# Kernel tuning notes

Hardware: AMD Instinct MI355X
Metric: run time of the kernel (lower is better)

## Reference

```python
import jax, jax.numpy as jnp
import numpy as np

H, W = 1024, 2048
NUM_POS_MAX, NUM_TOTAL = 32, 128
POS_THR, NEG_THR = 0.5, 0.5
B, G, R = 8, 256, 16384
N = R + G  # rois + appended gt boxes per image


def _xy2cxcy(xy):
    # NOTE: original code halves wh (divides by 2.0) -- kept faithfully.
    return jnp.concatenate([(xy[..., 2:] + xy[..., :2]) / 2.0,
                            (xy[..., 2:] - xy[..., :2]) / 2.0], axis=-1)


def _encode(gt_cxcy, anc_cxcy):
    tg_cxy = (gt_cxcy[..., :2] - anc_cxcy[..., :2]) / anc_cxcy[..., 2:]
    tg_wh = jnp.log(gt_cxcy[..., 2:] / anc_cxcy[..., 2:])
    return jnp.concatenate([tg_cxy, tg_wh], axis=-1)


def _rank(key_vals):
    # rank of each element when sorted ascending (stable)
    return jnp.argsort(jnp.argsort(key_vals))


def _sample_one(gt_bbox, gt_label, roi, rp, rn):
    scale = jnp.array([W, H, W, H], dtype=roi.dtype)
    allroi = jnp.concatenate([roi, gt_bbox / scale], axis=0)  # (N,4)
    # dense IoU matrix (N,G) -- the memory-bound core
    lb = jnp.maximum(allroi[:, None, :2], gt_bbox[None, :, :2])
    ub = jnp.minimum(allroi[:, None, 2:], gt_bbox[None, :, 2:])
    whi = jnp.clip(ub - lb, 0.0)
    inter = whi[..., 0] * whi[..., 1]
    a1 = jnp.clip((allroi[:, 2] - allroi[:, 0]) * (allroi[:, 3] - allroi[:, 1]), 0.0)[:, None]
    a2 = jnp.clip((gt_bbox[:, 2] - gt_bbox[:, 0]) * (gt_bbox[:, 3] - gt_bbox[:, 1]), 0.0)[None, :]
    iou = inter / (a1 + a2 - inter)
    iou_max = iou.max(axis=1)
    iou_argmax = iou.argmax(axis=1)
    label_all = gt_label[iou_argmax] + 1

    pos_mask = iou_max >= POS_THR
    neg_mask = (iou_max < NEG_THR) & (iou_max >= 0.0)
    num_pos = jnp.minimum(pos_mask.sum(), NUM_POS_MAX)
    num_neg = NUM_TOTAL - num_pos
    # random-subset selection via random-key ranking (replaces torch.randperm)
    pos_rank = _rank(jnp.where(pos_mask, rp, jnp.inf))
    neg_rank = _rank(jnp.where(neg_mask, rn, jnp.inf))
    sel_pos = pos_mask & (pos_rank < num_pos)
    sel_neg = neg_mask & (neg_rank < num_neg)
    # positives occupy slots [0,num_pos), negatives slots [num_pos,NUM_TOTAL)
    slot = jnp.where(sel_pos, pos_rank, jnp.where(sel_neg, num_pos + neg_rank, NUM_TOTAL))
    sampled_ids = jnp.zeros((NUM_TOTAL,), jnp.int32).at[slot].set(
        jnp.arange(N, dtype=jnp.int32), mode='drop')

    label = jnp.where(jnp.arange(NUM_TOTAL) < num_pos,
                      label_all[sampled_ids], 0).astype(jnp.int32)
    target_bbox = gt_bbox[iou_argmax][sampled_ids]
    sampled_roi = allroi[sampled_ids]
    std = jnp.array([0.1, 0.1, 0.2, 0.2], dtype=roi.dtype)
    encoded = _encode(_xy2cxcy(target_bbox), _xy2cxcy(sampled_roi)) / std
    return label, encoded, sampled_roi


def setup_inputs() -> dict:
    key = jax.random.key(0)
    ks = jax.random.split(key, 7)
    sxy = jnp.array([W, H], jnp.float32)
    gt_x1y1 = jax.random.uniform(ks[0], (B, G, 2)) * 0.8 * sxy
    gt_wh = jax.random.uniform(ks[1], (B, G, 2)) * 0.15 * sxy + 2.0
    gt_bboxes = jnp.concatenate([gt_x1y1, gt_x1y1 + gt_wh], axis=-1)
    gt_labels = jax.random.randint(ks[2], (B, G), 0, 80)
    r_x1y1 = jax.random.uniform(ks[3], (B, R, 2)) * 0.8
    r_wh = jax.random.uniform(ks[4], (B, R, 2)) * 0.15 + 0.002
    rois = jnp.concatenate([r_x1y1, r_x1y1 + r_wh], axis=-1)
    rand_pos = jax.random.uniform(ks[5], (B, N))
    rand_neg = jax.random.uniform(ks[6], (B, N))
    return {"gt_bboxes": gt_bboxes, "gt_labels": gt_labels, "rois": rois,
            "rand_pos": rand_pos, "rand_neg": rand_neg}


def reference(gt_bboxes, gt_labels, rois, rand_pos, rand_neg):
    labels, bboxes, sampled_rois = jax.vmap(_sample_one)(
        gt_bboxes, gt_labels, rois, rand_pos, rand_neg)
    return labels, bboxes, sampled_rois
```

## Files before the change

kernel.cpp:

```cpp
#include <hip/hip_runtime.h>
#include <stdint.h>

#define HH 1024
#define WW 2048
#define GG 256
#define RRN 16384
#define NN 16640
#define NV (NN / 4)
#define BB 8
#define NUM_POS_MAX 32
#define NUM_TOTAL 128
#define CAP 1024
#define SEL_T 1024

__global__ __launch_bounds__(256) void iou_kernel(const float* __restrict__ gt,
                                                  const float* __restrict__ rois,
                                                  uint32_t* __restrict__ codes) {
#pragma clang fp contract(off)
    __shared__ float4 sg[GG];
    __shared__ float sa2[GG];
    int b = blockIdx.x / 65;
    int chunk = blockIdx.x % 65;
    int tid = threadIdx.x;

    float4 g = reinterpret_cast<const float4*>(gt)[b * GG + tid];
    sg[tid] = g;
    sa2[tid] = fmaxf((g.z - g.x) * (g.w - g.y), 0.0f);
    __syncthreads();

    int i = chunk * 256 + tid;
    float4 rb;
    if (i < RRN) {
        rb = reinterpret_cast<const float4*>(rois)[b * RRN + i];
    } else {
        float4 gp = sg[i - RRN];
        rb = make_float4(gp.x / (float)WW, gp.y / (float)HH,
                         gp.z / (float)WW, gp.w / (float)HH);
    }
    float a1 = fmaxf((rb.z - rb.x) * (rb.w - rb.y), 0.0f);

    float best = -1.0f;
    int bestj = 0;
    for (int j = 0; j < GG; ++j) {
        float4 gj = sg[j];
        float lx = fmaxf(rb.x, gj.x);
        float ly = fmaxf(rb.y, gj.y);
        float ux = fminf(rb.z, gj.z);
        float uy = fminf(rb.w, gj.w);
        float iw = fmaxf(ux - lx, 0.0f);
        float ih = fmaxf(uy - ly, 0.0f);
        float inter = iw * ih;
        float denom = (a1 + sa2[j]) - inter;
        float iou = inter / denom;
        if (iou > best) { best = iou; bestj = j; }
    }

    bool pos = (best >= 0.5f);
    codes[b * NN + i] = (uint32_t)bestj | (pos ? 0x10000u : 0u);
}

__device__ __forceinline__ void write_sample(int b, int s, int mi, int np,
                                             const float* __restrict__ gt,
                                             const int* __restrict__ gl,
                                             const float* __restrict__ rois,
                                             const uint32_t* __restrict__ codes,
                                             float* __restrict__ out) {
#pragma clang fp contract(off)
    uint32_t code = codes[b * NN + mi];
    int amax = (int)(code & 0xFFFFu);
    int label = (s < np) ? (gl[b * GG + amax] + 1) : 0;

    float4 tb = reinterpret_cast<const float4*>(gt)[b * GG + amax];
    float4 ar;
    if (mi < RRN) {
        ar = reinterpret_cast<const float4*>(rois)[b * RRN + mi];
    } else {
        float4 gp = reinterpret_cast<const float4*>(gt)[b * GG + (mi - RRN)];
        ar = make_float4(gp.x / (float)WW, gp.y / (float)HH,
                         gp.z / (float)WW, gp.w / (float)HH);
    }

    float acx = (ar.z + ar.x) / 2.0f, acy = (ar.w + ar.y) / 2.0f;
    float aw  = (ar.z - ar.x) / 2.0f, ah  = (ar.w - ar.y) / 2.0f;
    float gcx = (tb.z + tb.x) / 2.0f, gcy = (tb.w + tb.y) / 2.0f;
    float gw  = (tb.z - tb.x) / 2.0f, gh  = (tb.w - tb.y) / 2.0f;

    float e0 = ((gcx - acx) / aw) / 0.1f;
    float e1 = ((gcy - acy) / ah) / 0.1f;
    float e2 = logf(gw / aw) / 0.2f;
    float e3 = logf(gh / ah) / 0.2f;

    int gid = b * NUM_TOTAL + s;
    out[gid] = (float)label;
    float* eo = out + BB * NUM_TOTAL + gid * 4;
    eo[0] = e0; eo[1] = e1; eo[2] = e2; eo[3] = e3;
    float* ro = out + BB * NUM_TOTAL + BB * NUM_TOTAL * 4 + gid * 4;
    ro[0] = ar.x; ro[1] = ar.y; ro[2] = ar.z; ro[3] = ar.w;
}

__global__ __launch_bounds__(SEL_T) void select_kernel(const uint32_t* __restrict__ codes,
                                                       const float* __restrict__ rp,
                                                       const float* __restrict__ rn,
                                                       const float* __restrict__ gt,
                                                       const int* __restrict__ gl,
                                                       const float* __restrict__ rois,
                                                       float* __restrict__ out) {
    __shared__ unsigned hist[1024];
    __shared__ uint32_t cbits[CAP];
    __shared__ int cidx[CAP];
    __shared__ int s_pc, s_cnt, s_k, s_np, s_p, s_total;

    int b = blockIdx.x >> 1;
    int t = blockIdx.x & 1;
    int tid = threadIdx.x;
    const float* rnd = (t == 0) ? rp : rn;
    const uint4* c4p = reinterpret_cast<const uint4*>(codes + b * NN);
    const float4* r4p = reinterpret_cast<const float4*>(rnd + b * NN);

    if (tid == 0) { s_pc = 0; s_cnt = 0; }
    __syncthreads();

    unsigned cutoff = 1000;
    for (int attempt = 0; attempt < 2; ++attempt) {
        hist[tid] = 0u;
        if (tid == 0) s_p = -1;
        __syncthreads();

        int myPos = 0;
        for (int v = tid; v < NV; v += SEL_T) {
            uint4 c4 = c4p[v];
            float4 r4 = r4p[v];
            uint32_t cc[4] = {c4.x, c4.y, c4.z, c4.w};
            float rr[4] = {r4.x, r4.y, r4.z, r4.w};
#pragma unroll
            for (int e = 0; e < 4; ++e) {
                bool isPos = (cc[e] & 0x10000u) != 0u;
                myPos += isPos ? 1 : 0;
                bool m = (t == 0) ? isPos : !isPos;
                if (m) {
                    unsigned bin = __float_as_uint(rr[e]) >> 20;
                    if (bin < cutoff) atomicAdd(&hist[bin], 1u);
                }
            }
        }
        if (attempt == 0) {
            for (int o = 32; o; o >>= 1) myPos += __shfl_down(myPos, o, 64);
            if ((tid & 63) == 0) atomicAdd(&s_pc, myPos);
        }
        __syncthreads();

        for (int off = 1; off < 1024; off <<= 1) {
            unsigned v = (tid >= off) ? hist[tid - off] : 0u;
            __syncthreads();
            hist[tid] += v;
            __syncthreads();
        }

        if (tid == 0) {
            int pc = s_pc;
            int np_ = min(pc, NUM_POS_MAX);
            int k = (t == 0) ? np_ : min(NN - pc, NUM_TOTAL - np_);
            s_np = np_;
            s_k = k;
            s_total = (int)hist[1023];
        }
        __syncthreads();

        int k = s_k;
        if (k > 0 && (int)hist[tid] >= k && (tid == 0 || (int)hist[tid - 1] < k))
            s_p = tid;
        __syncthreads();

        if (s_k == 0 || s_total >= s_k) break;
        cutoff = 1024;
    }

    int p = s_p;
    int k = s_k;
    int np_ = s_np;

    if (p >= 0) {
        for (int v = tid; v < NV; v += SEL_T) {
            uint4 c4 = c4p[v];
            float4 r4 = r4p[v];
            uint32_t cc[4] = {c4.x, c4.y, c4.z, c4.w};
            float rr[4] = {r4.x, r4.y, r4.z, r4.w};
#pragma unroll
            for (int e = 0; e < 4; ++e) {
                bool isPos = (cc[e] & 0x10000u) != 0u;
                bool m = (t == 0) ? isPos : !isPos;
                if (m) {
                    uint32_t bits = __float_as_uint(rr[e]);
                    if ((int)(bits >> 20) <= p) {
                        int ix = atomicAdd(&s_cnt, 1);
                        if (ix < CAP) { cbits[ix] = bits; cidx[ix] = v * 4 + e; }
                    }
                }
            }
        }
    }
    __syncthreads();

    int c = min(s_cnt, CAP);
    for (int ci = tid; ci < c; ci += SEL_T) {
        uint32_t mb = cbits[ci];
        int mi = cidx[ci];
        int r = 0;
        for (int j = 0; j < c; ++j) {
            uint32_t ob = cbits[j];
            r += ((ob < mb) || (ob == mb && cidx[j] < mi)) ? 1 : 0;
        }
        if (r < k) {
            int s = (t == 0) ? r : (np_ + r);
            write_sample(b, s, mi, np_, gt, gl, rois, codes, out);
        }
    }

    if (t == 1) {
        for (int s = np_ + k + tid; s < NUM_TOTAL; s += SEL_T)
            write_sample(b, s, 0, np_, gt, gl, rois, codes, out);
    }
}

extern "C" void kernel_launch(void* const* d_in, const int* in_sizes, int n_in,
                              void* d_out, int out_size, void* d_ws, size_t ws_size,
                              hipStream_t stream) {
    const float* gt   = (const float*)d_in[0];
    const int*   gl   = (const int*)d_in[1];
    const float* rois = (const float*)d_in[2];
    const float* rp   = (const float*)d_in[3];
    const float* rn   = (const float*)d_in[4];
    float* out = (float*)d_out;

    uint32_t* codes = (uint32_t*)d_ws;

    hipLaunchKernelGGL(iou_kernel, dim3(BB * 65), dim3(256), 0, stream,
                       gt, rois, codes);
    hipLaunchKernelGGL(select_kernel, dim3(BB * 2), dim3(SEL_T), 0, stream,
                       codes, rp, rn, gt, gl, rois, out);
}
```

Before: 114.2 us.

## Skip IoU division for non-overlapping boxes and add fast-path candidate selection

```diff
diff --git a/kernel.cpp b/kernel.cpp
--- a/kernel.cpp
+++ b/kernel.cpp
@@ -12,20 +12,18 @@
 #define NUM_TOTAL 128
 #define CAP 1024
 #define SEL_T 1024
+#define CUT_BITS 0x3C800000u
 
 __global__ __launch_bounds__(256) void iou_kernel(const float* __restrict__ gt,
                                                   const float* __restrict__ rois,
                                                   uint32_t* __restrict__ codes) {
 #pragma clang fp contract(off)
     __shared__ float4 sg[GG];
-    __shared__ float sa2[GG];
     int b = blockIdx.x / 65;
     int chunk = blockIdx.x % 65;
     int tid = threadIdx.x;
 
-    float4 g = reinterpret_cast<const float4*>(gt)[b * GG + tid];
-    sg[tid] = g;
-    sa2[tid] = fmaxf((g.z - g.x) * (g.w - g.y), 0.0f);
+    sg[tid] = reinterpret_cast<const float4*>(gt)[b * GG + tid];
     __syncthreads();
 
     int i = chunk * 256 + tid;
@@ -39,20 +37,35 @@
     }
     float a1 = fmaxf((rb.z - rb.x) * (rb.w - rb.y), 0.0f);
 
-    float best = -1.0f;
+    float best;
     int bestj = 0;
-    for (int j = 0; j < GG; ++j) {
+    {
+        float4 gj = sg[0];
+        float lx = fmaxf(rb.x, gj.x), ly = fmaxf(rb.y, gj.y);
+        float ux = fminf(rb.z, gj.z), uy = fminf(rb.w, gj.w);
+        float iw = fmaxf(ux - lx, 0.0f), ih = fmaxf(uy - ly, 0.0f);
+        float inter = iw * ih;
+        if (inter > 0.0f) {
+            float a2 = fmaxf((gj.z - gj.x) * (gj.w - gj.y), 0.0f);
+            float denom = (a1 + a2) - inter;
+            best = inter / denom;
+        } else {
+            best = 0.0f;
+        }
+    }
+#pragma unroll 4
+    for (int j = 1; j < GG; ++j) {
         float4 gj = sg[j];
-        float lx = fmaxf(rb.x, gj.x);
-        float ly = fmaxf(rb.y, gj.y);
-        float ux = fminf(rb.z, gj.z);
-        float uy = fminf(rb.w, gj.w);
-        float iw = fmaxf(ux - lx, 0.0f);
-        float ih = fmaxf(uy - ly, 0.0f);
+        float lx = fmaxf(rb.x, gj.x), ly = fmaxf(rb.y, gj.y);
+        float ux = fminf(rb.z, gj.z), uy = fminf(rb.w, gj.w);
+        float iw = fmaxf(ux - lx, 0.0f), ih = fmaxf(uy - ly, 0.0f);
         float inter = iw * ih;
-        float denom = (a1 + sa2[j]) - inter;
-        float iou = inter / denom;
-        if (iou > best) { best = iou; bestj = j; }
+        if (inter > 0.0f) {
+            float a2 = fmaxf((gj.z - gj.x) * (gj.w - gj.y), 0.0f);
+            float denom = (a1 + a2) - inter;
+            float iou = inter / denom;
+            if (iou > best) { best = iou; bestj = j; }
+        }
     }
 
     bool pos = (best >= 0.5f);
@@ -108,7 +121,7 @@
     __shared__ unsigned hist[1024];
     __shared__ uint32_t cbits[CAP];
     __shared__ int cidx[CAP];
-    __shared__ int s_pc, s_cnt, s_k, s_np, s_p, s_total;
+    __shared__ int s_pc, s_cnt, s_p;
 
     int b = blockIdx.x >> 1;
     int t = blockIdx.x & 1;
@@ -120,66 +133,40 @@
     if (tid == 0) { s_pc = 0; s_cnt = 0; }
     __syncthreads();
 
-    unsigned cutoff = 1000;
-    for (int attempt = 0; attempt < 2; ++attempt) {
-        hist[tid] = 0u;
-        if (tid == 0) s_p = -1;
-        __syncthreads();
-
-        int myPos = 0;
-        for (int v = tid; v < NV; v += SEL_T) {
-            uint4 c4 = c4p[v];
-            float4 r4 = r4p[v];
-            uint32_t cc[4] = {c4.x, c4.y, c4.z, c4.w};
-            float rr[4] = {r4.x, r4.y, r4.z, r4.w};
+    int myPos = 0;
+    for (int v = tid; v < NV; v += SEL_T) {
+        uint4 c4 = c4p[v];
+        float4 r4 = r4p[v];
+        uint32_t cc[4] = {c4.x, c4.y, c4.z, c4.w};
+        float rr[4] = {r4.x, r4.y, r4.z, r4.w};
 #pragma unroll
-            for (int e = 0; e < 4; ++e) {
-                bool isPos = (cc[e] & 0x10000u) != 0u;
-                myPos += isPos ? 1 : 0;
-                bool m = (t == 0) ? isPos : !isPos;
-                if (m) {
-                    unsigned bin = __float_as_uint(rr[e]) >> 20;
-                    if (bin < cutoff) atomicAdd(&hist[bin], 1u);
+        for (int e = 0; e < 4; ++e) {
+            bool isPos = (cc[e] & 0x10000u) != 0u;
+            myPos += isPos ? 1 : 0;
+            bool m = (t == 0) ? isPos : !isPos;
+            if (m) {
+                uint32_t bits = __float_as_uint(rr[e]);
+                if (bits < CUT_BITS) {
+                    int ix = atomicAdd(&s_cnt, 1);
+                    if (ix < CAP) { cbits[ix] = bits; cidx[ix] = v * 4 + e; }
                 }
             }
         }
-        if (attempt == 0) {
-            for (int o = 32; o; o >>= 1) myPos += __shfl_down(myPos, o, 64);
-            if ((tid & 63) == 0) atomicAdd(&s_pc, myPos);
-        }
-        __syncthreads();
-
-        for (int off = 1; off < 1024; off <<= 1) {
-            unsigned v = (tid >= off) ? hist[tid - off] : 0u;
-            __syncthreads();
-            hist[tid] += v;
-            __syncthreads();
-        }
-
-        if (tid == 0) {
-            int pc = s_pc;
-            int np_ = min(pc, NUM_POS_MAX);
-            int k = (t == 0) ? np_ : min(NN - pc, NUM_TOTAL - np_);
-            s_np = np_;
-            s_k = k;
-            s_total = (int)hist[1023];
-        }
-        __syncthreads();
-
-        int k = s_k;
-        if (k > 0 && (int)hist[tid] >= k && (tid == 0 || (int)hist[tid - 1] < k))
-            s_p = tid;
-        __syncthreads();
-
-        if (s_k == 0 || s_total >= s_k) break;
-        cutoff = 1024;
-    }
-
-    int p = s_p;
-    int k = s_k;
-    int np_ = s_np;
-
-    if (p >= 0) {
+    }
+    for (int o = 32; o; o >>= 1) myPos += __shfl_down(myPos, o, 64);
+    if ((tid & 63) == 0) atomicAdd(&s_pc, myPos);
+    __syncthreads();
+
+    int pc = s_pc;
+    int np_ = min(pc, NUM_POS_MAX);
+    int k = (t == 0) ? np_ : min(NN - pc, NUM_TOTAL - np_);
+    int total = s_cnt;
+    bool fast = (total >= k) && (total <= CAP);
+
+    if (!fast) {
+        hist[tid] = 0u;
+        if (tid == 0) { s_cnt = 0; s_p = -1; }
+        __syncthreads();
         for (int v = tid; v < NV; v += SEL_T) {
             uint4 c4 = c4p[v];
             float4 r4 = r4p[v];
@@ -189,17 +176,42 @@
             for (int e = 0; e < 4; ++e) {
                 bool isPos = (cc[e] & 0x10000u) != 0u;
                 bool m = (t == 0) ? isPos : !isPos;
-                if (m) {
-                    uint32_t bits = __float_as_uint(rr[e]);
-                    if ((int)(bits >> 20) <= p) {
-                        int ix = atomicAdd(&s_cnt, 1);
-                        if (ix < CAP) { cbits[ix] = bits; cidx[ix] = v * 4 + e; }
+                if (m) atomicAdd(&hist[__float_as_uint(rr[e]) >> 20], 1u);
+            }
+        }
+        __syncthreads();
+        for (int off = 1; off < 1024; off <<= 1) {
+            unsigned v = (tid >= off) ? hist[tid - off] : 0u;
+            __syncthreads();
+            hist[tid] += v;
+            __syncthreads();
+        }
+        if (k > 0 && (int)hist[tid] >= k && (tid == 0 || (int)hist[tid - 1] < k))
+            s_p = tid;
+        __syncthreads();
+        int p = s_p;
+        if (p >= 0) {
+            for (int v = tid; v < NV; v += SEL_T) {
+                uint4 c4 = c4p[v];
+                float4 r4 = r4p[v];
+                uint32_t cc[4] = {c4.x, c4.y, c4.z, c4.w};
+                float rr[4] = {r4.x, r4.y, r4.z, r4.w};
+#pragma unroll
+                for (int e = 0; e < 4; ++e) {
+                    bool isPos = (cc[e] & 0x10000u) != 0u;
+                    bool m = (t == 0) ? isPos : !isPos;
+                    if (m) {
+                        uint32_t bits = __float_as_uint(rr[e]);
+                        if ((int)(bits >> 20) <= p) {
+                            int ix = atomicAdd(&s_cnt, 1);
+                            if (ix < CAP) { cbits[ix] = bits; cidx[ix] = v * 4 + e; }
+                        }
                     }
                 }
             }
         }
-    }
-    __syncthreads();
+        __syncthreads();
+    }
 
     int c = min(s_cnt, CAP);
     for (int ci = tid; ci < c; ci += SEL_T) {
```

Result: faster. 103.5 us (-9.3%).
